# Performance work log

Measured on AMD Instinct MI355X. Metric: run time of the kernel, lower is better.

## Reference

```python
import jax, jax.numpy as jnp
import numpy as np

D_MODEL = 768
N_HEADS = 12
D_HEAD = D_MODEL // N_HEADS
B, L = 2, 4096


def setup_inputs() -> dict:
    key = jax.random.key(0)
    k1, k2, k3 = jax.random.split(key, 3)
    scale = 1.0 / np.sqrt(D_MODEL)
    return {
        "x": jax.random.normal(k1, (B, L, D_MODEL), dtype=jnp.float32),
        "w_qkv": jax.random.normal(k2, (D_MODEL, 3 * D_MODEL), dtype=jnp.float32) * scale,
        "b_qkv": jnp.zeros((3 * D_MODEL,), dtype=jnp.float32),
        "w_out": jax.random.normal(k3, (D_MODEL, D_MODEL), dtype=jnp.float32) * scale,
        "b_out": jnp.zeros((D_MODEL,), dtype=jnp.float32),
    }


def reference(x, w_qkv, b_qkv, w_out, b_out):
    b, l, d = x.shape
    # qkv projection -> (B, L, 3, H, Dh) -> split
    qkv = (x @ w_qkv + b_qkv).reshape(b, l, 3, N_HEADS, D_HEAD)
    qkv = jnp.transpose(qkv, (2, 0, 3, 1, 4))  # (3, B, H, L, Dh)
    q, k, v = qkv[0], qkv[1], qkv[2]
    # scaled scores with causal mask (dropout=0 / eval mode)
    att = jnp.einsum("bhqd,bhkd->bhqk", q, k) * (D_HEAD ** -0.5)
    causal = jnp.tril(jnp.ones((l, l), dtype=bool))
    att = jnp.where(causal, att, -jnp.inf)
    att = jax.nn.softmax(att, axis=-1)
    out = jnp.einsum("bhqk,bhkd->bhqd", att, v)  # (B, H, L, Dh)
    out = jnp.transpose(out, (0, 2, 1, 3)).reshape(b, l, d)
    return out @ w_out + b_out
```

## Files before the change

kernel.cpp:

```cpp
#include <hip/hip_runtime.h>
#include <hip/hip_bf16.h>

#define D_MODEL 768
#define NH 12
#define DHd 64
#define NB 2
#define SL 4096
#define BLr (NB*SL)
#define N3 (3*D_MODEL)
#define QSCALE 0.18033688011112042f

typedef __bf16 bf16x8 __attribute__((ext_vector_type(8)));
typedef float f32x4 __attribute__((ext_vector_type(4)));
typedef float f32x16 __attribute__((ext_vector_type(16)));
typedef unsigned int u32x4 __attribute__((ext_vector_type(4)));

__device__ __forceinline__ unsigned short f2bf(float f) {
  unsigned int u = __float_as_uint(f);
  u = (u + 0x7FFFu + ((u >> 16) & 1u)) >> 16;
  return (unsigned short)u;
}
__device__ __forceinline__ unsigned short bfc(float f) {
  __bf16 h = (__bf16)f;
  return __builtin_bit_cast(unsigned short, h);
}
__device__ __forceinline__ float fexp2(float x) {
  float r; asm("v_exp_f32 %0, %1" : "=v"(r) : "v"(x)); return r;
}
__device__ __forceinline__ unsigned int pk2(float lo, float hi2) {
  unsigned int r;
  asm("v_cvt_pk_bf16_f32 %0, %1, %2" : "=v"(r) : "v"(lo), "v"(hi2));
  return r;
}
__device__ __forceinline__ float vsum16(const f32x16& v) {
  float a = (v[0]+v[1])+(v[2]+v[3]);
  float b = (v[4]+v[5])+(v[6]+v[7]);
  float c = (v[8]+v[9])+(v[10]+v[11]);
  float d = (v[12]+v[13])+(v[14]+v[15]);
  return (a+b)+(c+d);
}
__device__ __forceinline__ void gload_lds16(const void* g, void* l) {
  __builtin_amdgcn_global_load_lds(
      (const __attribute__((address_space(1))) void*)g,
      (__attribute__((address_space(3))) void*)l, 16, 0, 0);
}

__global__ __launch_bounds__(256) void cast_f32_bf16(const float* __restrict__ in,
                                                     unsigned short* __restrict__ out, int n4) {
  int i = blockIdx.x * 256 + threadIdx.x;
  if (i >= n4) return;
  float4 v = reinterpret_cast<const float4*>(in)[i];
  ushort4 o;
  o.x = f2bf(v.x); o.y = f2bf(v.y); o.z = f2bf(v.z); o.w = f2bf(v.w);
  reinterpret_cast<ushort4*>(out)[i] = o;
}

__global__ __launch_bounds__(256) void transpose_cast(const float* __restrict__ in,
                                                      unsigned short* __restrict__ out,
                                                      int R, int C) {
  __shared__ float t[32][33];
  int c0 = blockIdx.x * 32, r0 = blockIdx.y * 32;
  int tx = threadIdx.x & 31, ty = threadIdx.x >> 5;
  #pragma unroll
  for (int i = 0; i < 32; i += 8) t[ty + i][tx] = in[(size_t)(r0 + ty + i) * C + c0 + tx];
  __syncthreads();
  #pragma unroll
  for (int i = 0; i < 32; i += 8) out[(size_t)(c0 + ty + i) * R + r0 + tx] = f2bf(t[tx][ty + i]);
}

template<int MODE>
__global__ __launch_bounds__(256) void gemm_bf16(const unsigned short* __restrict__ A,
                                                 const unsigned short* __restrict__ Bt,
                                                 const float* __restrict__ bias,
                                                 void* __restrict__ o0, void* __restrict__ o1,
                                                 void* __restrict__ o2,
                                                 int M, int N, int Kdim) {
  __shared__ unsigned short As[128 * 32];
  __shared__ unsigned short Bs[128 * 32];
  const int tid = threadIdx.x;
  const int lane = tid & 63, wave = tid >> 6;
  const int tm = blockIdx.x * 128, tn = blockIdx.y * 128;
  const int wm = (wave >> 1) * 64, wn = (wave & 1) * 64;
  const int fr = lane & 15, fk8 = (lane >> 4) * 8;
  const int srow = wave * 32 + (lane >> 2);
  const int scol = (lane & 3) * 8;

  f32x4 acc[4][4] = {};

  for (int k0 = 0; k0 < Kdim; k0 += 32) {
    __syncthreads();
    gload_lds16(A  + (size_t)(tm + srow)      * Kdim + k0 + scol, As + (wave * 32)      * 32);
    gload_lds16(A  + (size_t)(tm + srow + 16) * Kdim + k0 + scol, As + (wave * 32 + 16) * 32);
    gload_lds16(Bt + (size_t)(tn + srow)      * Kdim + k0 + scol, Bs + (wave * 32)      * 32);
    gload_lds16(Bt + (size_t)(tn + srow + 16) * Kdim + k0 + scol, Bs + (wave * 32 + 16) * 32);
    __syncthreads();

    bf16x8 af[4], bfr[4];
    #pragma unroll
    for (int i = 0; i < 4; i++) {
      af[i]  = *(const bf16x8*)(As + (wm + i * 16 + fr) * 32 + fk8);
      bfr[i] = *(const bf16x8*)(Bs + (wn + i * 16 + fr) * 32 + fk8);
    }
    #pragma unroll
    for (int i = 0; i < 4; i++)
      #pragma unroll
      for (int j = 0; j < 4; j++)
        acc[i][j] = __builtin_amdgcn_mfma_f32_16x16x32_bf16(af[i], bfr[j], acc[i][j], 0, 0, 0);
  }

  const int fq = (lane >> 4) * 4;
  if constexpr (MODE == 0) {
    unsigned short* Qf = (unsigned short*)o0;
    unsigned short* Kf = (unsigned short*)o1;
    unsigned short* Vf = (unsigned short*)o2;
    #pragma unroll
    for (int j = 0; j < 4; j++) {
      int col = tn + wn + j * 16 + fr;
      float bv = bias[col];
      int which = col / D_MODEL;
      int hd = col % D_MODEL;
      int h = hd >> 6, d = hd & 63;
      #pragma unroll
      for (int i = 0; i < 4; i++) {
        #pragma unroll
        for (int r = 0; r < 4; r++) {
          int row = tm + wm + i * 16 + fq + r;
          int b = row >> 12, l = row & 4095;
          float v = acc[i][j][r] + bv;
          size_t hb = (size_t)b * NH + h;
          if (which == 2) {
            size_t off = ((hb * 64 + (l >> 6)) * 8 + ((l >> 4) & 3) * 2 + (d >> 5)) * 512
                       + (size_t)((d & 31) + 32 * ((l >> 2) & 1)) * 8
                       + ((l & 3) + 4 * ((l >> 3) & 1));
            Vf[off] = bfc(v);
          } else {
            size_t off = ((hb * 128 + (l >> 5)) * 4 + (d >> 4)) * 512
                       + (size_t)((l & 31) + 32 * ((d >> 3) & 1)) * 8 + (d & 7);
            if (which == 0) Qf[off] = bfc(v * QSCALE);
            else            Kf[off] = bfc(v);
          }
        }
      }
    }
  } else {
    float* Out = (float*)o0;
    #pragma unroll
    for (int i = 0; i < 4; i++)
      #pragma unroll
      for (int j = 0; j < 4; j++) {
        int col = tn + wn + j * 16 + fr;
        float bv = bias[col];
        #pragma unroll
        for (int r = 0; r < 4; r++) {
          int row = tm + wm + i * 16 + fq + r;
          Out[(size_t)row * N + col] = acc[i][j][r] + bv;
        }
      }
  }
}

#define PVSTEP(P, B, VB0, VB1) do {                                        \
    u32x4 w4;                                                              \
    w4[0] = pk2(P[(B)+0], P[(B)+1]);                                       \
    w4[1] = pk2(P[(B)+2], P[(B)+3]);                                       \
    w4[2] = pk2(P[(B)+4], P[(B)+5]);                                       \
    w4[3] = pk2(P[(B)+6], P[(B)+7]);                                       \
    bf16x8 pa = __builtin_bit_cast(bf16x8, w4);                            \
    oacc0 = __builtin_amdgcn_mfma_f32_32x32x16_bf16(pa, VB0, oacc0, 0,0,0);\
    oacc1 = __builtin_amdgcn_mfma_f32_32x32x16_bf16(pa, VB1, oacc1, 0,0,0);\
  } while(0)

__global__ __launch_bounds__(128) void attn_fwd(const unsigned short* __restrict__ Qf,
                                                const unsigned short* __restrict__ Kf,
                                                const unsigned short* __restrict__ Vf,
                                                unsigned short* __restrict__ O) {
  const int bid = blockIdx.x;
  const int t = 63 - (bid / 48);
  const int r48 = bid % 48;
  const int bh = r48 % 24;
  const int s = r48 / 24;
  const int tid = threadIdx.x;
  const int w = tid >> 6;
  const int lane = tid & 63;
  const int l31 = lane & 31, hi = lane >> 5;
  const int Cm1 = 2 * t + s;

  __shared__ float LoA[16][64];
  __shared__ float LoB[16][64];
  __shared__ float Ll[64];

  const char* Kbh = (const char*)Kf + ((size_t)bh * 512) * 1024 + lane * 16;
  const char* Vbh = (const char*)Vf + ((size_t)bh * 512) * 1024 + lane * 16;
  const int b = bh / NH, h = bh % NH;

  bf16x8 qf[4];
  const char* Qb_ = (const char*)Qf + (((size_t)bh * 128 + t * 2 + s) * 4) * 1024 + lane * 16;
  #pragma unroll
  for (int f = 0; f < 4; f++) qf[f] = *(const bf16x8*)(Qb_ + f * 1024);

  f32x16 oacc0 = {}, oacc1 = {};
  float l_i = 0.f;

  for (int c = w; c <= Cm1; c += 2) {
    const char* kp = Kbh + (size_t)c * 4096;
    bf16x8 kf0 = *(const bf16x8*)(kp);
    bf16x8 kf1 = *(const bf16x8*)(kp + 1024);
    bf16x8 kf2 = *(const bf16x8*)(kp + 2048);
    bf16x8 kf3 = *(const bf16x8*)(kp + 3072);
    const char* vp = Vbh + (size_t)c * 4096;
    bf16x8 v0a = *(const bf16x8*)(vp);
    bf16x8 v0b = *(const bf16x8*)(vp + 1024);

    f32x16 sS;
    #pragma unroll
    for (int r = 0; r < 16; r++) sS[r] = -16.0f;

    __builtin_amdgcn_s_setprio(1);
    sS = __builtin_amdgcn_mfma_f32_32x32x16_bf16(kf0, qf[0], sS, 0, 0, 0);
    sS = __builtin_amdgcn_mfma_f32_32x32x16_bf16(kf1, qf[1], sS, 0, 0, 0);
    sS = __builtin_amdgcn_mfma_f32_32x32x16_bf16(kf2, qf[2], sS, 0, 0, 0);
    sS = __builtin_amdgcn_mfma_f32_32x32x16_bf16(kf3, qf[3], sS, 0, 0, 0);
    __builtin_amdgcn_s_setprio(0);

    if (c == Cm1) {
      #pragma unroll
      for (int r = 0; r < 16; r++) {
        int kvo = (r & 3) + 8 * (r >> 2) + 4 * hi;
        if (kvo > l31) sS[r] = -1e30f;
      }
    }

    #pragma unroll
    for (int r = 0; r < 16; r++) sS[r] = fexp2(sS[r]);
    float ts = vsum16(sS);
    ts += __shfl_xor(ts, 32);
    l_i += ts;

    __builtin_amdgcn_s_setprio(1);
    PVSTEP(sS, 0, v0a, v0b);
    {
      bf16x8 v1a = *(const bf16x8*)(vp + 2048);
      bf16x8 v1b = *(const bf16x8*)(vp + 3072);
      PVSTEP(sS, 8, v1a, v1b);
    }
    __builtin_amdgcn_s_setprio(0);
  }

  if (w == 1) {
    #pragma unroll
    for (int r = 0; r < 16; r++) {
      LoA[r][lane] = oacc0[r];
      LoB[r][lane] = oacc1[r];
    }
    Ll[lane] = l_i;
  }
  __syncthreads();

  if (w == 0) {
    float lm = l_i + Ll[lane];
    const int q0w = t * 64 + s * 32;
    #pragma unroll
    for (int r = 0; r < 16; r++) {
      int qo = (r & 3) + 8 * (r >> 2) + 4 * hi;
      float linv = 1.0f / __shfl(lm, qo);
      float o0 = (oacc0[r] + LoA[r][lane]) * linv;
      float o1 = (oacc1[r] + LoB[r][lane]) * linv;
      size_t base = ((size_t)b * SL + q0w + qo) * D_MODEL + h * DHd;
      O[base + l31]      = bfc(o0);
      O[base + 32 + l31] = bfc(o1);
    }
  }
}

extern "C" void kernel_launch(void* const* d_in, const int* in_sizes, int n_in,
                              void* d_out, int out_size, void* d_ws, size_t ws_size,
                              hipStream_t stream) {
  (void)in_sizes; (void)n_in; (void)out_size; (void)ws_size;
  const float* x     = (const float*)d_in[0];
  const float* w_qkv = (const float*)d_in[1];
  const float* b_qkv = (const float*)d_in[2];
  const float* w_out = (const float*)d_in[3];
  const float* b_out = (const float*)d_in[4];
  float* out = (float*)d_out;

  unsigned short* p = (unsigned short*)d_ws;
  unsigned short* xb    = p; p += (size_t)BLr * D_MODEL;
  unsigned short* wqkvT = p; p += (size_t)N3 * D_MODEL;
  unsigned short* woutT = p; p += (size_t)D_MODEL * D_MODEL;
  unsigned short* Qf    = p; p += (size_t)NB * NH * SL * DHd;
  unsigned short* Kf    = p; p += (size_t)NB * NH * SL * DHd;
  unsigned short* Vf    = p; p += (size_t)NB * NH * SL * DHd;
  unsigned short* Ob    = p;

  cast_f32_bf16<<<(BLr * D_MODEL / 4 + 255) / 256, 256, 0, stream>>>(x, xb, BLr * D_MODEL / 4);
  transpose_cast<<<dim3(N3 / 32, D_MODEL / 32), 256, 0, stream>>>(w_qkv, wqkvT, D_MODEL, N3);
  transpose_cast<<<dim3(D_MODEL / 32, D_MODEL / 32), 256, 0, stream>>>(w_out, woutT, D_MODEL, D_MODEL);
  gemm_bf16<0><<<dim3(BLr / 128, N3 / 128), 256, 0, stream>>>(xb, wqkvT, b_qkv, Qf, Kf, Vf,
                                                              BLr, N3, D_MODEL);
  attn_fwd<<<3072, 128, 0, stream>>>(Qf, Kf, Vf, Ob);
  gemm_bf16<1><<<dim3(BLr / 128, D_MODEL / 128), 256, 0, stream>>>(Ob, woutT, b_out, out,
                                                                   nullptr, nullptr,
                                                                   BLr, D_MODEL, D_MODEL);
}
```

Baseline: 178.7 us.

## Merge weight transposes, retile output GEMM, compute softmax row sums via MFMA

The two weight transpose-cast launches are merged into one kernel. The output projection GEMM now uses 128x64 tiles with 2 waves, doubling the block count to fill more CUs. In attention, the per-tile scalar row-sum reduction (vsum16 plus a shuffle) becomes an extra MFMA against a ones vector, which moves that work onto the matrix unit. The fixed -16 score offset is dropped, so scores start at zero. Without that offset exp2 may overflow for large scores, and the extra MFMA adds matrix-unit work to each tile.

```diff
diff --git a/kernel.cpp b/kernel.cpp
--- a/kernel.cpp
+++ b/kernel.cpp
@@ -32,13 +32,6 @@
   asm("v_cvt_pk_bf16_f32 %0, %1, %2" : "=v"(r) : "v"(lo), "v"(hi2));
   return r;
 }
-__device__ __forceinline__ float vsum16(const f32x16& v) {
-  float a = (v[0]+v[1])+(v[2]+v[3]);
-  float b = (v[4]+v[5])+(v[6]+v[7]);
-  float c = (v[8]+v[9])+(v[10]+v[11]);
-  float d = (v[12]+v[13])+(v[14]+v[15]);
-  return (a+b)+(c+d);
-}
 __device__ __forceinline__ void gload_lds16(const void* g, void* l) {
   __builtin_amdgcn_global_load_lds(
       (const __attribute__((address_space(1))) void*)g,
@@ -55,11 +48,16 @@
   reinterpret_cast<ushort4*>(out)[i] = o;
 }
 
-__global__ __launch_bounds__(256) void transpose_cast(const float* __restrict__ in,
-                                                      unsigned short* __restrict__ out,
-                                                      int R, int C) {
+__global__ __launch_bounds__(256) void transpose_cast2(const float* __restrict__ wq,
+                                                       unsigned short* __restrict__ oq,
+                                                       const float* __restrict__ wo,
+                                                       unsigned short* __restrict__ oo) {
   __shared__ float t[32][33];
-  int c0 = blockIdx.x * 32, r0 = blockIdx.y * 32;
+  const int bx = blockIdx.x;
+  const float* in; unsigned short* out; int R, C, c0;
+  if (bx < 72) { in = wq; out = oq; R = 768; C = 2304; c0 = bx * 32; }
+  else         { in = wo; out = oo; R = 768; C = 768;  c0 = (bx - 72) * 32; }
+  int r0 = blockIdx.y * 32;
   int tx = threadIdx.x & 31, ty = threadIdx.x >> 5;
   #pragma unroll
   for (int i = 0; i < 32; i += 8) t[ty + i][tx] = in[(size_t)(r0 + ty + i) * C + c0 + tx];
@@ -68,13 +66,13 @@
   for (int i = 0; i < 32; i += 8) out[(size_t)(c0 + ty + i) * R + r0 + tx] = f2bf(t[tx][ty + i]);
 }
 
-template<int MODE>
-__global__ __launch_bounds__(256) void gemm_bf16(const unsigned short* __restrict__ A,
-                                                 const unsigned short* __restrict__ Bt,
-                                                 const float* __restrict__ bias,
-                                                 void* __restrict__ o0, void* __restrict__ o1,
-                                                 void* __restrict__ o2,
-                                                 int M, int N, int Kdim) {
+__global__ __launch_bounds__(256) void gemm_qkv(const unsigned short* __restrict__ A,
+                                                const unsigned short* __restrict__ Bt,
+                                                const float* __restrict__ bias,
+                                                unsigned short* __restrict__ Qf,
+                                                unsigned short* __restrict__ Kf,
+                                                unsigned short* __restrict__ Vf,
+                                                int M, int N, int Kdim) {
   __shared__ unsigned short As[128 * 32];
   __shared__ unsigned short Bs[128 * 32];
   const int tid = threadIdx.x;
@@ -109,54 +107,91 @@
   }
 
   const int fq = (lane >> 4) * 4;
-  if constexpr (MODE == 0) {
-    unsigned short* Qf = (unsigned short*)o0;
-    unsigned short* Kf = (unsigned short*)o1;
-    unsigned short* Vf = (unsigned short*)o2;
-    #pragma unroll
-    for (int j = 0; j < 4; j++) {
-      int col = tn + wn + j * 16 + fr;
-      float bv = bias[col];
-      int which = col / D_MODEL;
-      int hd = col % D_MODEL;
-      int h = hd >> 6, d = hd & 63;
-      #pragma unroll
-      for (int i = 0; i < 4; i++) {
-        #pragma unroll
-        for (int r = 0; r < 4; r++) {
-          int row = tm + wm + i * 16 + fq + r;
-          int b = row >> 12, l = row & 4095;
-          float v = acc[i][j][r] + bv;
-          size_t hb = (size_t)b * NH + h;
-          if (which == 2) {
-            size_t off = ((hb * 64 + (l >> 6)) * 8 + ((l >> 4) & 3) * 2 + (d >> 5)) * 512
-                       + (size_t)((d & 31) + 32 * ((l >> 2) & 1)) * 8
-                       + ((l & 3) + 4 * ((l >> 3) & 1));
-            Vf[off] = bfc(v);
-          } else {
-            size_t off = ((hb * 128 + (l >> 5)) * 4 + (d >> 4)) * 512
-                       + (size_t)((l & 31) + 32 * ((d >> 3) & 1)) * 8 + (d & 7);
-            if (which == 0) Qf[off] = bfc(v * QSCALE);
-            else            Kf[off] = bfc(v);
-          }
+  #pragma unroll
+  for (int j = 0; j < 4; j++) {
+    int col = tn + wn + j * 16 + fr;
+    float bv = bias[col];
+    int which = col / D_MODEL;
+    int hd = col % D_MODEL;
+    int h = hd >> 6, d = hd & 63;
+    #pragma unroll
+    for (int i = 0; i < 4; i++) {
+      #pragma unroll
+      for (int r = 0; r < 4; r++) {
+        int row = tm + wm + i * 16 + fq + r;
+        int b = row >> 12, l = row & 4095;
+        float v = acc[i][j][r] + bv;
+        size_t hb = (size_t)b * NH + h;
+        if (which == 2) {
+          size_t off = ((hb * 64 + (l >> 6)) * 8 + ((l >> 4) & 3) * 2 + (d >> 5)) * 512
+                     + (size_t)((d & 31) + 32 * ((l >> 2) & 1)) * 8
+                     + ((l & 3) + 4 * ((l >> 3) & 1));
+          Vf[off] = bfc(v);
+        } else {
+          size_t off = ((hb * 128 + (l >> 5)) * 4 + (d >> 4)) * 512
+                     + (size_t)((l & 31) + 32 * ((d >> 3) & 1)) * 8 + (d & 7);
+          if (which == 0) Qf[off] = bfc(v * QSCALE);
+          else            Kf[off] = bfc(v);
         }
       }
     }
-  } else {
-    float* Out = (float*)o0;
+  }
+}
+
+__global__ __launch_bounds__(128) void gemm_out(const unsigned short* __restrict__ A,
+                                                const unsigned short* __restrict__ Bt,
+                                                const float* __restrict__ bias,
+                                                float* __restrict__ Out,
+                                                int M, int N, int Kdim) {
+  __shared__ unsigned short As[128 * 32];
+  __shared__ unsigned short Bs[64 * 32];
+  const int tid = threadIdx.x;
+  const int lane = tid & 63, wave = tid >> 6;
+  const int tm = blockIdx.x * 128, tn = blockIdx.y * 64;
+  const int wm = wave * 64;
+  const int fr = lane & 15, fk8 = (lane >> 4) * 8;
+  const int srA = wave * 64 + (lane >> 2);
+  const int srB = wave * 32 + (lane >> 2);
+  const int scol = (lane & 3) * 8;
+
+  f32x4 acc[4][4] = {};
+
+  for (int k0 = 0; k0 < Kdim; k0 += 32) {
+    __syncthreads();
+    gload_lds16(A  + (size_t)(tm + srA)      * Kdim + k0 + scol, As + (wave * 64)      * 32);
+    gload_lds16(A  + (size_t)(tm + srA + 16) * Kdim + k0 + scol, As + (wave * 64 + 16) * 32);
+    gload_lds16(A  + (size_t)(tm + srA + 32) * Kdim + k0 + scol, As + (wave * 64 + 32) * 32);
+    gload_lds16(A  + (size_t)(tm + srA + 48) * Kdim + k0 + scol, As + (wave * 64 + 48) * 32);
+    gload_lds16(Bt + (size_t)(tn + srB)      * Kdim + k0 + scol, Bs + (wave * 32)      * 32);
+    gload_lds16(Bt + (size_t)(tn + srB + 16) * Kdim + k0 + scol, Bs + (wave * 32 + 16) * 32);
+    __syncthreads();
+
+    bf16x8 af[4], bfr[4];
+    #pragma unroll
+    for (int i = 0; i < 4; i++) {
+      af[i]  = *(const bf16x8*)(As + (wm + i * 16 + fr) * 32 + fk8);
+      bfr[i] = *(const bf16x8*)(Bs + (i * 16 + fr) * 32 + fk8);
+    }
     #pragma unroll
     for (int i = 0; i < 4; i++)
       #pragma unroll
-      for (int j = 0; j < 4; j++) {
-        int col = tn + wn + j * 16 + fr;
-        float bv = bias[col];
-        #pragma unroll
-        for (int r = 0; r < 4; r++) {
-          int row = tm + wm + i * 16 + fq + r;
-          Out[(size_t)row * N + col] = acc[i][j][r] + bv;
-        }
+      for (int j = 0; j < 4; j++)
+        acc[i][j] = __builtin_amdgcn_mfma_f32_16x16x32_bf16(af[i], bfr[j], acc[i][j], 0, 0, 0);
+  }
+
+  const int fq = (lane >> 4) * 4;
+  #pragma unroll
+  for (int i = 0; i < 4; i++)
+    #pragma unroll
+    for (int j = 0; j < 4; j++) {
+      int col = tn + j * 16 + fr;
+      float bv = bias[col];
+      #pragma unroll
+      for (int r = 0; r < 4; r++) {
+        int row = tm + wm + i * 16 + fq + r;
+        Out[(size_t)row * N + col] = acc[i][j][r] + bv;
       }
-  }
+    }
 }
 
 #define PVSTEP(P, B, VB0, VB1) do {                                        \
@@ -168,6 +203,7 @@
     bf16x8 pa = __builtin_bit_cast(bf16x8, w4);                            \
     oacc0 = __builtin_amdgcn_mfma_f32_32x32x16_bf16(pa, VB0, oacc0, 0,0,0);\
     oacc1 = __builtin_amdgcn_mfma_f32_32x32x16_bf16(pa, VB1, oacc1, 0,0,0);\
+    lacc  = __builtin_amdgcn_mfma_f32_32x32x16_bf16(pa, onesB, lacc, 0,0,0);\
   } while(0)
 
 __global__ __launch_bounds__(128) void attn_fwd(const unsigned short* __restrict__ Qf,
@@ -187,7 +223,7 @@
 
   __shared__ float LoA[16][64];
   __shared__ float LoB[16][64];
-  __shared__ float Ll[64];
+  __shared__ float Lsum[2][32];
 
   const char* Kbh = (const char*)Kf + ((size_t)bh * 512) * 1024 + lane * 16;
   const char* Vbh = (const char*)Vf + ((size_t)bh * 512) * 1024 + lane * 16;
@@ -198,8 +234,12 @@
   #pragma unroll
   for (int f = 0; f < 4; f++) qf[f] = *(const bf16x8*)(Qb_ + f * 1024);
 
-  f32x16 oacc0 = {}, oacc1 = {};
-  float l_i = 0.f;
+  unsigned int ow = (l31 == 0) ? 0x3F803F80u : 0u;
+  u32x4 o4; o4[0] = ow; o4[1] = ow; o4[2] = ow; o4[3] = ow;
+  const bf16x8 onesB = __builtin_bit_cast(bf16x8, o4);
+
+  f32x16 zf = {};
+  f32x16 oacc0 = {}, oacc1 = {}, lacc = {};
 
   for (int c = w; c <= Cm1; c += 2) {
     const char* kp = Kbh + (size_t)c * 4096;
@@ -211,12 +251,8 @@
     bf16x8 v0a = *(const bf16x8*)(vp);
     bf16x8 v0b = *(const bf16x8*)(vp + 1024);
 
-    f32x16 sS;
-    #pragma unroll
-    for (int r = 0; r < 16; r++) sS[r] = -16.0f;
-
     __builtin_amdgcn_s_setprio(1);
-    sS = __builtin_amdgcn_mfma_f32_32x32x16_bf16(kf0, qf[0], sS, 0, 0, 0);
+    f32x16 sS = __builtin_amdgcn_mfma_f32_32x32x16_bf16(kf0, qf[0], zf, 0, 0, 0);
     sS = __builtin_amdgcn_mfma_f32_32x32x16_bf16(kf1, qf[1], sS, 0, 0, 0);
     sS = __builtin_amdgcn_mfma_f32_32x32x16_bf16(kf2, qf[2], sS, 0, 0, 0);
     sS = __builtin_amdgcn_mfma_f32_32x32x16_bf16(kf3, qf[3], sS, 0, 0, 0);
@@ -232,9 +268,6 @@
 
     #pragma unroll
     for (int r = 0; r < 16; r++) sS[r] = fexp2(sS[r]);
-    float ts = vsum16(sS);
-    ts += __shfl_xor(ts, 32);
-    l_i += ts;
 
     __builtin_amdgcn_s_setprio(1);
     PVSTEP(sS, 0, v0a, v0b);
@@ -246,18 +279,22 @@
     __builtin_amdgcn_s_setprio(0);
   }
 
+  if (l31 == 0) {
+    #pragma unroll
+    for (int r = 0; r < 16; r++)
+      Lsum[w][(r & 3) + 8 * (r >> 2) + 4 * hi] = lacc[r];
+  }
   if (w == 1) {
     #pragma unroll
     for (int r = 0; r < 16; r++) {
       LoA[r][lane] = oacc0[r];
       LoB[r][lane] = oacc1[r];
     }
-    Ll[lane] = l_i;
   }
   __syncthreads();
 
   if (w == 0) {
-    float lm = l_i + Ll[lane];
+    float lm = Lsum[0][l31] + Lsum[1][l31];
     const int q0w = t * 64 + s * 32;
     #pragma unroll
     for (int r = 0; r < 16; r++) {
@@ -293,12 +330,10 @@
   unsigned short* Ob    = p;
 
   cast_f32_bf16<<<(BLr * D_MODEL / 4 + 255) / 256, 256, 0, stream>>>(x, xb, BLr * D_MODEL / 4);
-  transpose_cast<<<dim3(N3 / 32, D_MODEL / 32), 256, 0, stream>>>(w_qkv, wqkvT, D_MODEL, N3);
-  transpose_cast<<<dim3(D_MODEL / 32, D_MODEL / 32), 256, 0, stream>>>(w_out, woutT, D_MODEL, D_MODEL);
-  gemm_bf16<0><<<dim3(BLr / 128, N3 / 128), 256, 0, stream>>>(xb, wqkvT, b_qkv, Qf, Kf, Vf,
-                                                              BLr, N3, D_MODEL);
+  transpose_cast2<<<dim3(96, 24), 256, 0, stream>>>(w_qkv, wqkvT, w_out, woutT);
+  gemm_qkv<<<dim3(BLr / 128, N3 / 128), 256, 0, stream>>>(xb, wqkvT, b_qkv, Qf, Kf, Vf,
+                                                          BLr, N3, D_MODEL);
   attn_fwd<<<3072, 128, 0, stream>>>(Qf, Kf, Vf, Ob);
-  gemm_bf16<1><<<dim3(BLr / 128, D_MODEL / 128), 256, 0, stream>>>(Ob, woutT, b_out, out,
-                                                                   nullptr, nullptr,
-                                                                   BLr, D_MODEL, D_MODEL);
-}
+  gemm_out<<<dim3(BLr / 128, D_MODEL / 64), 128, 0, stream>>>(Ob, woutT, b_out, out,
+                                                              BLr, D_MODEL, D_MODEL);
+}
```

Result: no change. 175.7 us (-1.7%).
